# Optimization experiments

Measured on AMD Instinct MI355X. Metric: run time of the kernel, lower is better.

The kernel has to match this reference:

```python
import jax, jax.numpy as jnp
import numpy as np

N = 131072      # nodes decoded per call
LAT, REP, H = 64, 128, 256
FEAT, CEMB, NMAP, CNUM = 512, 128, 101, 27
TEMP = 0.5


def setup_inputs() -> dict:
    key = jax.random.key(0)
    ks = iter(jax.random.split(key, 40))
    w = lambda shape: jax.random.normal(next(ks), shape, jnp.float32) * 0.02
    inp = {
        "z": jax.random.normal(next(ks), (N, LAT), jnp.float32),
        "cluster_ind": jax.random.randint(next(ks), (N,), 0, CNUM),
        "Emb": w((CNUM, CEMB)),
        "Wld": w((LAT, REP)), "bld": w((REP,)),
        "Wrd": w((REP, 3 * H)), "brd": w((3 * H,)),
        "Wfd": w((H, FEAT)), "bfd": w((FEAT,)),
        "Wc1": w((H, H)), "bc1": w((H,)),
        "Wc2": w((H, H)), "bc2": w((H,)),
        "Wc3": w((H, H)), "bc3": w((H,)),
        "Wcd": w((H, CNUM)), "bcd": w((CNUM,)),
        "Wcn": w((CEMB, H)), "bcn": w((H,)),
        "Wnd": w((H, 2 * H)), "bnd": w((2 * H,)),
        "Wn1": w((2 * H, 2 * H)), "bn1": w((2 * H,)),
        "Wn2": w((2 * H, 2 * H)), "bn2": w((2 * H,)),
        "Wa0": w((2 * H, 4 * H)), "ba0": w((4 * H,)),
        "Wa1": w((4 * H, 2 * H)), "ba1": w((2 * H,)),
        "Wn3": w((2 * H, NMAP)), "bn3": w((NMAP,)),
    }
    return inp


def reference(z, cluster_ind, Emb, Wld, bld, Wrd, brd, Wfd, bfd,
              Wc1, bc1, Wc2, bc2, Wc3, bc3, Wcd, bcd, Wcn, bcn,
              Wnd, bnd, Wn1, bn1, Wn2, bn2, Wa0, ba0, Wa1, ba1, Wn3, bn3):
    relu = jax.nn.relu
    # latent -> reparam -> hidden*3, chunked into (feat, neighbor, cluster)
    z1 = relu(z @ Wld + bld)
    z2 = relu(z1 @ Wrd + brd)
    feat_h, nb_h, cl_h = jnp.split(z2, 3, axis=-1)  # each [N, H]
    # feature head
    feat = jax.nn.sigmoid(feat_h @ Wfd + bfd)
    # cluster head
    c = relu(cl_h @ Wc1 + bc1)
    c = relu(c @ Wc2 + bc2)
    c = relu(c @ Wc3 + bc3)
    cluster = jax.nn.sigmoid((c @ Wcd + bcd) / TEMP)
    # neighbor head, conditioned on cluster embedding (training branch)
    emb = Emb[cluster_ind]                      # [N, CEMB]
    ctn = relu(emb @ Wcn + bcn)                 # [N, H]
    nf = relu((nb_h + ctn) @ Wnd + bnd)
    nf = relu(nf @ Wn1 + bn1)
    nf = relu(nf @ Wn2 + bn2)
    nf = relu(nf @ Wa0 + ba0)
    nf = relu(nf @ Wa1 + ba1)
    neighbor_map = jax.nn.sigmoid((nf @ Wn3 + bn3) / TEMP)
    return (feat, neighbor_map, cluster)
```

## Files before the change

kernel.cpp:

```cpp
#include <hip/hip_runtime.h>
#include <hip/hip_bf16.h>

typedef short bf16x8 __attribute__((ext_vector_type(8)));
typedef float f32x4 __attribute__((ext_vector_type(4)));

#define NN 131072
#define BM 128
#define WRS 512
#define SRS 128

#define OFF_LD 0
#define OFF_RD 8192
#define OFF_FD 106496
#define OFF_C1 237568
#define OFF_C2 303104
#define OFF_C3 368640
#define OFF_CD 434176
#define OFF_CN 442368
#define OFF_ND 475136
#define OFF_N1 606208
#define OFF_N2 868352
#define OFF_A0 1130496
#define OFF_A1 1654784
#define OFF_N3 2179072
#define WT_TOTAL 2236416

__device__ __forceinline__ unsigned short f2b(float f) {
  __hip_bfloat16 h = __float2bfloat16(f);
  return __builtin_bit_cast(unsigned short, h);
}
__device__ __forceinline__ float b2f(unsigned short u) {
  return __bfloat162float(__builtin_bit_cast(__hip_bfloat16, u));
}

template<int Kd, int Md>
__device__ __forceinline__ unsigned short convF(int local, const float* __restrict__ W) {
  int block = local >> 9;
  int within = local & 511;
  int lane = within >> 3, j = within & 7;
  constexpr int NK = Kd / 32;
  int ctile = block / NK;
  int kch = block - ctile * NK;
  int col = ctile * 16 + (lane & 15);
  int k = kch * 32 + (lane >> 4) * 8 + j;
  return (col < Md) ? f2b(W[(size_t)k * Md + col]) : (unsigned short)0;
}

__global__ void prep_weights(const float* __restrict__ Wld, const float* __restrict__ Wrd,
                             const float* __restrict__ Wfd, const float* __restrict__ Wc1,
                             const float* __restrict__ Wc2, const float* __restrict__ Wc3,
                             const float* __restrict__ Wcd, const float* __restrict__ Wcn,
                             const float* __restrict__ Wnd, const float* __restrict__ Wn1,
                             const float* __restrict__ Wn2, const float* __restrict__ Wa0,
                             const float* __restrict__ Wa1, const float* __restrict__ Wn3,
                             unsigned short* __restrict__ WT) {
  int e = blockIdx.x * 256 + threadIdx.x;
  unsigned short r;
  if      (e < OFF_RD) r = convF<64, 128>(e - OFF_LD, Wld);
  else if (e < OFF_FD) r = convF<128, 768>(e - OFF_RD, Wrd);
  else if (e < OFF_C1) r = convF<256, 512>(e - OFF_FD, Wfd);
  else if (e < OFF_C2) r = convF<256, 256>(e - OFF_C1, Wc1);
  else if (e < OFF_C3) r = convF<256, 256>(e - OFF_C2, Wc2);
  else if (e < OFF_CD) r = convF<256, 256>(e - OFF_C3, Wc3);
  else if (e < OFF_CN) r = convF<256, 27>(e - OFF_CD, Wcd);
  else if (e < OFF_ND) r = convF<128, 256>(e - OFF_CN, Wcn);
  else if (e < OFF_N1) r = convF<256, 512>(e - OFF_ND, Wnd);
  else if (e < OFF_N2) r = convF<512, 512>(e - OFF_N1, Wn1);
  else if (e < OFF_A0) r = convF<512, 512>(e - OFF_N2, Wn2);
  else if (e < OFF_A1) r = convF<512, 1024>(e - OFF_A0, Wa0);
  else if (e < OFF_N3) r = convF<1024, 512>(e - OFF_A1, Wa1);
  else                 r = convF<512, 101>(e - OFF_N3, Wn3);
  WT[e] = r;
}

template<int K, int NOUT, int GSIZE, int ACT, bool TO_GLOBAL, bool ADD>
__device__ __forceinline__ void layer(
    const unsigned short* __restrict__ Ain, int ars,
    const unsigned short* __restrict__ Bw,
    const float* __restrict__ bias,
    unsigned short* __restrict__ Lout, int ors,
    float* __restrict__ Gout, int gld,
    const unsigned short* __restrict__ Aadd, int rsa,
    int lane, int wid) {
  constexpr int NS = K / 32;
  constexpr int NT = (NOUT + 15) >> 4;
  constexpr int NG = (NT + GSIZE - 1) / GSIZE;
  const int l15 = lane & 15;
  const int quad = lane >> 4;
  const int kh = quad << 3;
  const int sw = (l15 & 7) << 3;
  const unsigned short* a0b = Ain + l15 * ars;
  const unsigned short* a1b = Ain + (64 + l15) * ars;
  #pragma unroll 1
  for (int g = wid; g < NG; g += 8) {
    f32x4 acc[8][GSIZE] = {};
    const unsigned short* bp[GSIZE];
    #pragma unroll
    for (int t = 0; t < GSIZE; ++t)
      bp[t] = Bw + (size_t)(g * GSIZE + t) * (NS * 512) + lane * 8;
    __builtin_amdgcn_s_setprio(1);
    #pragma unroll 2
    for (int s = 0; s < NS; ++s) {
      bf16x8 bb[GSIZE];
      #pragma unroll
      for (int t = 0; t < GSIZE; ++t) bb[t] = *(const bf16x8*)(bp[t] + s * 512);
      int kx = (kh + s * 32) ^ sw;
      #pragma unroll
      for (int m = 0; m < 8; ++m) {
        bf16x8 a = *(const bf16x8*)((m < 4 ? a0b : a1b) + (m & 3) * 16 * ars + kx);
        #pragma unroll
        for (int t = 0; t < GSIZE; ++t)
          acc[m][t] = __builtin_amdgcn_mfma_f32_16x16x32_bf16(a, bb[t], acc[m][t], 0, 0, 0);
      }
    }
    __builtin_amdgcn_s_setprio(0);
    #pragma unroll
    for (int t = 0; t < GSIZE; ++t) {
      int col = (g * GSIZE + t) * 16 + l15;
      int cc = col < NOUT ? col : NOUT - 1;
      float bb2 = bias[cc];
      #pragma unroll
      for (int m = 0; m < 8; ++m) {
        #pragma unroll
        for (int j = 0; j < 4; ++j) {
          int row = m * 16 + quad * 4 + j;
          int rsw = (row & 7) << 3;
          float v = acc[m][t][j] + bb2;
          if constexpr (ACT == 0) v = fmaxf(v, 0.f);
          else if constexpr (ACT == 1) v = 1.f / (1.f + __expf(-v));
          else if constexpr (ACT == 2) v = 1.f / (1.f + __expf(-2.f * v));
          if constexpr (ADD) v += b2f(Aadd[row * rsa + (col ^ rsw)]);
          if constexpr (TO_GLOBAL) {
            if (col < NOUT) Gout[(size_t)row * gld + col] = v;
          } else {
            Lout[row * ors + (col ^ rsw)] = f2b(v);
          }
        }
      }
    }
  }
}

template<int K>
__device__ __forceinline__ void layer512_ip(
    unsigned short* __restrict__ Wb,
    const unsigned short* __restrict__ Bw, const float* __restrict__ bias,
    int lane, int wid) {
  constexpr int NS = K / 32;
  const int l15 = lane & 15;
  const int quad = lane >> 4;
  const int kh = quad << 3;
  const int sw = (l15 & 7) << 3;
  f32x4 acc[8][4] = {};
  const unsigned short* bp[4];
  #pragma unroll
  for (int t = 0; t < 4; ++t)
    bp[t] = Bw + (size_t)(wid * 4 + t) * (NS * 512) + lane * 8;
  const unsigned short* a0b = Wb + l15 * WRS;
  const unsigned short* a1b = Wb + (64 + l15) * WRS;
  __builtin_amdgcn_s_setprio(1);
  #pragma unroll 2
  for (int s = 0; s < NS; ++s) {
    bf16x8 bb[4];
    #pragma unroll
    for (int t = 0; t < 4; ++t) bb[t] = *(const bf16x8*)(bp[t] + s * 512);
    int kx = (kh + s * 32) ^ sw;
    #pragma unroll
    for (int m = 0; m < 8; ++m) {
      bf16x8 a = *(const bf16x8*)((m < 4 ? a0b : a1b) + (m & 3) * 16 * WRS + kx);
      #pragma unroll
      for (int t = 0; t < 4; ++t)
        acc[m][t] = __builtin_amdgcn_mfma_f32_16x16x32_bf16(a, bb[t], acc[m][t], 0, 0, 0);
    }
  }
  __builtin_amdgcn_s_setprio(0);
  __syncthreads();
  #pragma unroll
  for (int t = 0; t < 4; ++t) {
    int col = wid * 64 + t * 16 + l15;
    float bb2 = bias[col];
    #pragma unroll
    for (int m = 0; m < 8; ++m) {
      #pragma unroll
      for (int j = 0; j < 4; ++j) {
        int row = m * 16 + quad * 4 + j;
        Wb[row * WRS + (col ^ ((row & 7) << 3))] = f2b(fmaxf(acc[m][t][j] + bb2, 0.f));
      }
    }
  }
  __syncthreads();
}

__global__ __launch_bounds__(512, 2)
void fused_vae(const float* __restrict__ z, const int* __restrict__ cind,
               const float* __restrict__ Emb,
               const float* __restrict__ bld, const float* __restrict__ brd,
               const float* __restrict__ bfd, const float* __restrict__ bc1,
               const float* __restrict__ bc2, const float* __restrict__ bc3,
               const float* __restrict__ bcd, const float* __restrict__ bcn,
               const float* __restrict__ bnd, const float* __restrict__ bn1,
               const float* __restrict__ bn2, const float* __restrict__ ba0,
               const float* __restrict__ ba1, const float* __restrict__ bn3,
               const unsigned short* __restrict__ WT, float* __restrict__ out) {
  __shared__ unsigned short lds[BM * (WRS + SRS)];
  unsigned short* Wb = lds;
  unsigned short* Sb = lds + BM * WRS;
  const int tid = threadIdx.x;
  const int lane = tid & 63;
  const int wid = tid >> 6;
  const size_t row0 = (size_t)blockIdx.x * BM;

  for (int e = tid * 4; e < BM * 64; e += 512 * 4) {
    int r = e >> 6, c = e & 63;
    float4 v = *(const float4*)(z + (row0 + r) * 64 + c);
    ushort4 u; u.x = f2b(v.x); u.y = f2b(v.y); u.z = f2b(v.z); u.w = f2b(v.w);
    *(ushort4*)(&Wb[r * WRS + (c ^ ((r & 7) << 3))]) = u;
  }
  __syncthreads();
  layer<64, 128, 1, 0, false, false>(Wb, WRS, WT + OFF_LD, bld, Sb, SRS, nullptr, 0, nullptr, 0, lane, wid);
  __syncthreads();
  layer<128, 256, 2, 0, false, false>(Sb, SRS, WT + OFF_RD + (size_t)32 * 4 * 512, brd + 512, Wb, WRS, nullptr, 0, nullptr, 0, lane, wid);
  __syncthreads();
  layer<256, 256, 2, 0, false, false>(Wb, WRS, WT + OFF_C1, bc1, Wb + 256, WRS, nullptr, 0, nullptr, 0, lane, wid);
  __syncthreads();
  layer<256, 256, 2, 0, false, false>(Wb + 256, WRS, WT + OFF_C2, bc2, Wb, WRS, nullptr, 0, nullptr, 0, lane, wid);
  __syncthreads();
  layer<256, 256, 2, 0, false, false>(Wb, WRS, WT + OFF_C3, bc3, Wb + 256, WRS, nullptr, 0, nullptr, 0, lane, wid);
  __syncthreads();
  layer<256, 27, 1, 2, true, false>(Wb + 256, WRS, WT + OFF_CD, bcd, nullptr, 0,
                                    out + (size_t)NN * 613 + row0 * 27, 27, nullptr, 0, lane, wid);
  layer<128, 256, 2, 0, false, false>(Sb, SRS, WT + OFF_RD, brd, Wb, WRS, nullptr, 0, nullptr, 0, lane, wid);
  __syncthreads();
  layer<256, 512, 2, 1, true, false>(Wb, WRS, WT + OFF_FD, bfd, nullptr, 0,
                                     out + row0 * 512, 512, nullptr, 0, lane, wid);
  layer<128, 256, 2, 0, false, false>(Sb, SRS, WT + OFF_RD + (size_t)16 * 4 * 512, brd + 256, Wb + 256, WRS, nullptr, 0, nullptr, 0, lane, wid);
  __syncthreads();
  for (int e = tid * 4; e < BM * 128; e += 512 * 4) {
    int r = e >> 7, c = e & 127;
    int ci = cind[row0 + r];
    float4 v = *(const float4*)(Emb + (size_t)ci * 128 + c);
    ushort4 u; u.x = f2b(v.x); u.y = f2b(v.y); u.z = f2b(v.z); u.w = f2b(v.w);
    *(ushort4*)(&Sb[r * SRS + (c ^ ((r & 7) << 3))]) = u;
  }
  __syncthreads();
  layer<128, 256, 2, 0, false, true>(Sb, SRS, WT + OFF_CN, bcn, Wb, WRS, nullptr, 0, Wb + 256, WRS, lane, wid);
  __syncthreads();
  layer512_ip<256>(Wb, WT + OFF_ND, bnd, lane, wid);
  layer512_ip<512>(Wb, WT + OFF_N1, bn1, lane, wid);
  layer512_ip<512>(Wb, WT + OFF_N2, bn2, lane, wid);
  {
    const int l15 = lane & 15;
    const int quad = lane >> 4;
    const int kh = quad << 3;
    const int sw = (l15 & 7) << 3;
    #pragma unroll 1
    for (int rh = 0; rh < 2; ++rh) {
      f32x4 acc1[4][4] = {};
      const unsigned short* awb = Wb + (rh * 64 + l15) * WRS;
      #pragma unroll 1
      for (int e = 0; e < 8; ++e) {
        unsigned short* sbuf = Sb + (e & 1) * (64 * SRS);
        f32x4 acc0[4] = {};
        const unsigned short* bp = WT + OFF_A0 + (size_t)(e * 8 + wid) * (16 * 512) + lane * 8;
        __builtin_amdgcn_s_setprio(1);
        #pragma unroll 2
        for (int s = 0; s < 16; ++s) {
          bf16x8 b = *(const bf16x8*)(bp + s * 512);
          int kx = (kh + s * 32) ^ sw;
          #pragma unroll
          for (int m = 0; m < 4; ++m) {
            bf16x8 a = *(const bf16x8*)(awb + m * 16 * WRS + kx);
            acc0[m] = __builtin_amdgcn_mfma_f32_16x16x32_bf16(a, b, acc0[m], 0, 0, 0);
          }
        }
        __builtin_amdgcn_s_setprio(0);
        {
          int lc = wid * 16 + l15;
          float bb2 = ba0[e * 128 + lc];
          #pragma unroll
          for (int m = 0; m < 4; ++m) {
            #pragma unroll
            for (int j = 0; j < 4; ++j) {
              int row = m * 16 + quad * 4 + j;
              sbuf[row * SRS + (lc ^ ((row & 7) << 3))] = f2b(fmaxf(acc0[m][j] + bb2, 0.f));
            }
          }
        }
        __syncthreads();
        const unsigned short* asb = sbuf + l15 * SRS;
        const unsigned short* bp1[4];
        #pragma unroll
        for (int t = 0; t < 4; ++t)
          bp1[t] = WT + OFF_A1 + (size_t)(wid * 4 + t) * (32 * 512) + (size_t)(e * 4) * 512 + lane * 8;
        __builtin_amdgcn_s_setprio(1);
        #pragma unroll
        for (int s = 0; s < 4; ++s) {
          bf16x8 b[4];
          #pragma unroll
          for (int t = 0; t < 4; ++t) b[t] = *(const bf16x8*)(bp1[t] + s * 512);
          int kx = (kh + s * 32) ^ sw;
          #pragma unroll
          for (int m = 0; m < 4; ++m) {
            bf16x8 a = *(const bf16x8*)(asb + m * 16 * SRS + kx);
            #pragma unroll
            for (int t = 0; t < 4; ++t)
              acc1[m][t] = __builtin_amdgcn_mfma_f32_16x16x32_bf16(a, b[t], acc1[m][t], 0, 0, 0);
          }
        }
        __builtin_amdgcn_s_setprio(0);
      }
      #pragma unroll
      for (int t = 0; t < 4; ++t) {
        int col = wid * 64 + t * 16 + l15;
        float bb2 = ba1[col];
        #pragma unroll
        for (int m = 0; m < 4; ++m) {
          #pragma unroll
          for (int j = 0; j < 4; ++j) {
            int row = rh * 64 + m * 16 + quad * 4 + j;
            Wb[row * WRS + (col ^ ((row & 7) << 3))] = f2b(fmaxf(acc1[m][t][j] + bb2, 0.f));
          }
        }
      }
    }
  }
  __syncthreads();
  layer<512, 101, 1, 2, true, false>(Wb, WRS, WT + OFF_N3, bn3, nullptr, 0,
                                     out + (size_t)NN * 512 + row0 * 101, 101, nullptr, 0, lane, wid);
}

extern "C" void kernel_launch(void* const* d_in, const int* in_sizes, int n_in,
                              void* d_out, int out_size, void* d_ws, size_t ws_size,
                              hipStream_t stream) {
  const float* z   = (const float*)d_in[0];
  const int*   cind= (const int*)d_in[1];
  const float* Emb = (const float*)d_in[2];
  const float* Wld = (const float*)d_in[3];  const float* bld = (const float*)d_in[4];
  const float* Wrd = (const float*)d_in[5];  const float* brd = (const float*)d_in[6];
  const float* Wfd = (const float*)d_in[7];  const float* bfd = (const float*)d_in[8];
  const float* Wc1 = (const float*)d_in[9];  const float* bc1 = (const float*)d_in[10];
  const float* Wc2 = (const float*)d_in[11]; const float* bc2 = (const float*)d_in[12];
  const float* Wc3 = (const float*)d_in[13]; const float* bc3 = (const float*)d_in[14];
  const float* Wcd = (const float*)d_in[15]; const float* bcd = (const float*)d_in[16];
  const float* Wcn = (const float*)d_in[17]; const float* bcn = (const float*)d_in[18];
  const float* Wnd = (const float*)d_in[19]; const float* bnd = (const float*)d_in[20];
  const float* Wn1 = (const float*)d_in[21]; const float* bn1 = (const float*)d_in[22];
  const float* Wn2 = (const float*)d_in[23]; const float* bn2 = (const float*)d_in[24];
  const float* Wa0 = (const float*)d_in[25]; const float* ba0 = (const float*)d_in[26];
  const float* Wa1 = (const float*)d_in[27]; const float* ba1 = (const float*)d_in[28];
  const float* Wn3 = (const float*)d_in[29]; const float* bn3 = (const float*)d_in[30];
  unsigned short* WT = (unsigned short*)d_ws;
  float* out = (float*)d_out;

  prep_weights<<<WT_TOTAL / 256, 256, 0, stream>>>(Wld, Wrd, Wfd, Wc1, Wc2, Wc3, Wcd,
                                                   Wcn, Wnd, Wn1, Wn2, Wa0, Wa1, Wn3, WT);
  fused_vae<<<NN / BM, 512, 0, stream>>>(z, cind, Emb, bld, brd, bfd, bc1, bc2, bc3,
                                         bcd, bcn, bnd, bn1, bn2, ba0, ba1, bn3, WT, out);
}
```

Measured before the change: 740.6 us.

## Split warps across row halves and widen column groups to cut weight reloads

The 8 warps are reorganized into 4 column groups by 2 row halves. Each warp now computes 64 rows by a wider set of output tiles (GSIZE doubled), so B-weight fragments loaded from global are reused across more MFMAs per A load. The fused A0/A1 MLP loop now processes 256-column chunks in 4 iterations with a single 64x256 staging buffer and an extra barrier, in place of 8 double-buffered 128-column chunks. This trades more accumulator registers and different LDS access patterns for fewer global weight fetches and fewer synchronisations.

```diff
diff --git a/kernel.cpp b/kernel.cpp
--- a/kernel.cpp
+++ b/kernel.cpp
@@ -85,19 +85,23 @@
   constexpr int NS = K / 32;
   constexpr int NT = (NOUT + 15) >> 4;
   constexpr int NG = (NT + GSIZE - 1) / GSIZE;
+  const int cg = wid >> 1;
+  const int rbase = (wid & 1) * 64;
   const int l15 = lane & 15;
   const int quad = lane >> 4;
   const int kh = quad << 3;
   const int sw = (l15 & 7) << 3;
-  const unsigned short* a0b = Ain + l15 * ars;
-  const unsigned short* a1b = Ain + (64 + l15) * ars;
+  const unsigned short* ab = Ain + (rbase + l15) * ars;
   #pragma unroll 1
-  for (int g = wid; g < NG; g += 8) {
-    f32x4 acc[8][GSIZE] = {};
+  for (int g = cg; g < NG; g += 4) {
+    f32x4 acc[4][GSIZE] = {};
     const unsigned short* bp[GSIZE];
     #pragma unroll
-    for (int t = 0; t < GSIZE; ++t)
-      bp[t] = Bw + (size_t)(g * GSIZE + t) * (NS * 512) + lane * 8;
+    for (int t = 0; t < GSIZE; ++t) {
+      int ti = g * GSIZE + t;
+      int tc = ti < NT ? ti : NT - 1;
+      bp[t] = Bw + (size_t)tc * (NS * 512) + lane * 8;
+    }
     __builtin_amdgcn_s_setprio(1);
     #pragma unroll 2
     for (int s = 0; s < NS; ++s) {
@@ -106,8 +110,8 @@
       for (int t = 0; t < GSIZE; ++t) bb[t] = *(const bf16x8*)(bp[t] + s * 512);
       int kx = (kh + s * 32) ^ sw;
       #pragma unroll
-      for (int m = 0; m < 8; ++m) {
-        bf16x8 a = *(const bf16x8*)((m < 4 ? a0b : a1b) + (m & 3) * 16 * ars + kx);
+      for (int m = 0; m < 4; ++m) {
+        bf16x8 a = *(const bf16x8*)(ab + m * 16 * ars + kx);
         #pragma unroll
         for (int t = 0; t < GSIZE; ++t)
           acc[m][t] = __builtin_amdgcn_mfma_f32_16x16x32_bf16(a, bb[t], acc[m][t], 0, 0, 0);
@@ -120,10 +124,10 @@
       int cc = col < NOUT ? col : NOUT - 1;
       float bb2 = bias[cc];
       #pragma unroll
-      for (int m = 0; m < 8; ++m) {
+      for (int m = 0; m < 4; ++m) {
         #pragma unroll
         for (int j = 0; j < 4; ++j) {
-          int row = m * 16 + quad * 4 + j;
+          int row = rbase + m * 16 + quad * 4 + j;
           int rsw = (row & 7) << 3;
           float v = acc[m][t][j] + bb2;
           if constexpr (ACT == 0) v = fmaxf(v, 0.f);
@@ -147,43 +151,41 @@
     const unsigned short* __restrict__ Bw, const float* __restrict__ bias,
     int lane, int wid) {
   constexpr int NS = K / 32;
+  const int cg = wid >> 1;
+  const int rbase = (wid & 1) * 64;
   const int l15 = lane & 15;
   const int quad = lane >> 4;
   const int kh = quad << 3;
   const int sw = (l15 & 7) << 3;
-  f32x4 acc[8][4] = {};
-  const unsigned short* bp[4];
-  #pragma unroll
-  for (int t = 0; t < 4; ++t)
-    bp[t] = Bw + (size_t)(wid * 4 + t) * (NS * 512) + lane * 8;
-  const unsigned short* a0b = Wb + l15 * WRS;
-  const unsigned short* a1b = Wb + (64 + l15) * WRS;
+  f32x4 acc[4][8] = {};
+  const unsigned short* bp = Bw + (size_t)(cg * 8) * (NS * 512) + lane * 8;
+  const unsigned short* ab = Wb + (rbase + l15) * WRS;
   __builtin_amdgcn_s_setprio(1);
   #pragma unroll 2
   for (int s = 0; s < NS; ++s) {
-    bf16x8 bb[4];
-    #pragma unroll
-    for (int t = 0; t < 4; ++t) bb[t] = *(const bf16x8*)(bp[t] + s * 512);
+    bf16x8 bb[8];
+    #pragma unroll
+    for (int t = 0; t < 8; ++t) bb[t] = *(const bf16x8*)(bp + (size_t)t * (NS * 512) + s * 512);
     int kx = (kh + s * 32) ^ sw;
     #pragma unroll
-    for (int m = 0; m < 8; ++m) {
-      bf16x8 a = *(const bf16x8*)((m < 4 ? a0b : a1b) + (m & 3) * 16 * WRS + kx);
-      #pragma unroll
-      for (int t = 0; t < 4; ++t)
+    for (int m = 0; m < 4; ++m) {
+      bf16x8 a = *(const bf16x8*)(ab + m * 16 * WRS + kx);
+      #pragma unroll
+      for (int t = 0; t < 8; ++t)
         acc[m][t] = __builtin_amdgcn_mfma_f32_16x16x32_bf16(a, bb[t], acc[m][t], 0, 0, 0);
     }
   }
   __builtin_amdgcn_s_setprio(0);
   __syncthreads();
   #pragma unroll
-  for (int t = 0; t < 4; ++t) {
-    int col = wid * 64 + t * 16 + l15;
+  for (int t = 0; t < 8; ++t) {
+    int col = cg * 128 + t * 16 + l15;
     float bb2 = bias[col];
     #pragma unroll
-    for (int m = 0; m < 8; ++m) {
+    for (int m = 0; m < 4; ++m) {
       #pragma unroll
       for (int j = 0; j < 4; ++j) {
-        int row = m * 16 + quad * 4 + j;
+        int row = rbase + m * 16 + quad * 4 + j;
         Wb[row * WRS + (col ^ ((row & 7) << 3))] = f2b(fmaxf(acc[m][t][j] + bb2, 0.f));
       }
     }
@@ -217,23 +219,23 @@
     *(ushort4*)(&Wb[r * WRS + (c ^ ((r & 7) << 3))]) = u;
   }
   __syncthreads();
-  layer<64, 128, 1, 0, false, false>(Wb, WRS, WT + OFF_LD, bld, Sb, SRS, nullptr, 0, nullptr, 0, lane, wid);
-  __syncthreads();
-  layer<128, 256, 2, 0, false, false>(Sb, SRS, WT + OFF_RD + (size_t)32 * 4 * 512, brd + 512, Wb, WRS, nullptr, 0, nullptr, 0, lane, wid);
-  __syncthreads();
-  layer<256, 256, 2, 0, false, false>(Wb, WRS, WT + OFF_C1, bc1, Wb + 256, WRS, nullptr, 0, nullptr, 0, lane, wid);
-  __syncthreads();
-  layer<256, 256, 2, 0, false, false>(Wb + 256, WRS, WT + OFF_C2, bc2, Wb, WRS, nullptr, 0, nullptr, 0, lane, wid);
-  __syncthreads();
-  layer<256, 256, 2, 0, false, false>(Wb, WRS, WT + OFF_C3, bc3, Wb + 256, WRS, nullptr, 0, nullptr, 0, lane, wid);
+  layer<64, 128, 2, 0, false, false>(Wb, WRS, WT + OFF_LD, bld, Sb, SRS, nullptr, 0, nullptr, 0, lane, wid);
+  __syncthreads();
+  layer<128, 256, 4, 0, false, false>(Sb, SRS, WT + OFF_RD + (size_t)32 * 4 * 512, brd + 512, Wb, WRS, nullptr, 0, nullptr, 0, lane, wid);
+  __syncthreads();
+  layer<256, 256, 4, 0, false, false>(Wb, WRS, WT + OFF_C1, bc1, Wb + 256, WRS, nullptr, 0, nullptr, 0, lane, wid);
+  __syncthreads();
+  layer<256, 256, 4, 0, false, false>(Wb + 256, WRS, WT + OFF_C2, bc2, Wb, WRS, nullptr, 0, nullptr, 0, lane, wid);
+  __syncthreads();
+  layer<256, 256, 4, 0, false, false>(Wb, WRS, WT + OFF_C3, bc3, Wb + 256, WRS, nullptr, 0, nullptr, 0, lane, wid);
   __syncthreads();
   layer<256, 27, 1, 2, true, false>(Wb + 256, WRS, WT + OFF_CD, bcd, nullptr, 0,
                                     out + (size_t)NN * 613 + row0 * 27, 27, nullptr, 0, lane, wid);
-  layer<128, 256, 2, 0, false, false>(Sb, SRS, WT + OFF_RD, brd, Wb, WRS, nullptr, 0, nullptr, 0, lane, wid);
-  __syncthreads();
-  layer<256, 512, 2, 1, true, false>(Wb, WRS, WT + OFF_FD, bfd, nullptr, 0,
+  layer<128, 256, 4, 0, false, false>(Sb, SRS, WT + OFF_RD, brd, Wb, WRS, nullptr, 0, nullptr, 0, lane, wid);
+  __syncthreads();
+  layer<256, 512, 4, 1, true, false>(Wb, WRS, WT + OFF_FD, bfd, nullptr, 0,
                                      out + row0 * 512, 512, nullptr, 0, lane, wid);
-  layer<128, 256, 2, 0, false, false>(Sb, SRS, WT + OFF_RD + (size_t)16 * 4 * 512, brd + 256, Wb + 256, WRS, nullptr, 0, nullptr, 0, lane, wid);
+  layer<128, 256, 4, 0, false, false>(Sb, SRS, WT + OFF_RD + (size_t)16 * 4 * 512, brd + 256, Wb + 256, WRS, nullptr, 0, nullptr, 0, lane, wid);
   __syncthreads();
   for (int e = tid * 4; e < BM * 128; e += 512 * 4) {
     int r = e >> 7, c = e & 127;
@@ -243,7 +245,7 @@
     *(ushort4*)(&Sb[r * SRS + (c ^ ((r & 7) << 3))]) = u;
   }
   __syncthreads();
-  layer<128, 256, 2, 0, false, true>(Sb, SRS, WT + OFF_CN, bcn, Wb, WRS, nullptr, 0, Wb + 256, WRS, lane, wid);
+  layer<128, 256, 4, 0, false, true>(Sb, SRS, WT + OFF_CN, bcn, Wb, WRS, nullptr, 0, Wb + 256, WRS, lane, wid);
   __syncthreads();
   layer512_ip<256>(Wb, WT + OFF_ND, bnd, lane, wid);
   layer512_ip<512>(Wb, WT + OFF_N1, bn1, lane, wid);
@@ -257,51 +259,51 @@
     for (int rh = 0; rh < 2; ++rh) {
       f32x4 acc1[4][4] = {};
       const unsigned short* awb = Wb + (rh * 64 + l15) * WRS;
+      const unsigned short* asb = Sb + l15 * 256;
       #pragma unroll 1
-      for (int e = 0; e < 8; ++e) {
-        unsigned short* sbuf = Sb + (e & 1) * (64 * SRS);
-        f32x4 acc0[4] = {};
-        const unsigned short* bp = WT + OFF_A0 + (size_t)(e * 8 + wid) * (16 * 512) + lane * 8;
+      for (int e = 0; e < 4; ++e) {
+        f32x4 acc0[4][2] = {};
+        const unsigned short* bp0 = WT + OFF_A0 + (size_t)(e * 16 + wid * 2) * (16 * 512) + lane * 8;
         __builtin_amdgcn_s_setprio(1);
         #pragma unroll 2
         for (int s = 0; s < 16; ++s) {
-          bf16x8 b = *(const bf16x8*)(bp + s * 512);
+          bf16x8 b0 = *(const bf16x8*)(bp0 + s * 512);
+          bf16x8 b1 = *(const bf16x8*)(bp0 + 16 * 512 + s * 512);
           int kx = (kh + s * 32) ^ sw;
           #pragma unroll
           for (int m = 0; m < 4; ++m) {
             bf16x8 a = *(const bf16x8*)(awb + m * 16 * WRS + kx);
-            acc0[m] = __builtin_amdgcn_mfma_f32_16x16x32_bf16(a, b, acc0[m], 0, 0, 0);
+            acc0[m][0] = __builtin_amdgcn_mfma_f32_16x16x32_bf16(a, b0, acc0[m][0], 0, 0, 0);
+            acc0[m][1] = __builtin_amdgcn_mfma_f32_16x16x32_bf16(a, b1, acc0[m][1], 0, 0, 0);
           }
         }
         __builtin_amdgcn_s_setprio(0);
-        {
-          int lc = wid * 16 + l15;
-          float bb2 = ba0[e * 128 + lc];
+        __syncthreads();
+        #pragma unroll
+        for (int t = 0; t < 2; ++t) {
+          int lc = wid * 32 + t * 16 + l15;
+          float bb2 = ba0[e * 256 + lc];
           #pragma unroll
           for (int m = 0; m < 4; ++m) {
             #pragma unroll
             for (int j = 0; j < 4; ++j) {
               int row = m * 16 + quad * 4 + j;
-              sbuf[row * SRS + (lc ^ ((row & 7) << 3))] = f2b(fmaxf(acc0[m][j] + bb2, 0.f));
+              Sb[row * 256 + (lc ^ ((row & 7) << 3))] = f2b(fmaxf(acc0[m][t][j] + bb2, 0.f));
             }
           }
         }
         __syncthreads();
-        const unsigned short* asb = sbuf + l15 * SRS;
-        const unsigned short* bp1[4];
-        #pragma unroll
-        for (int t = 0; t < 4; ++t)
-          bp1[t] = WT + OFF_A1 + (size_t)(wid * 4 + t) * (32 * 512) + (size_t)(e * 4) * 512 + lane * 8;
+        const unsigned short* bp1 = WT + OFF_A1 + (size_t)(wid * 4) * (32 * 512) + (size_t)(e * 8) * 512 + lane * 8;
         __builtin_amdgcn_s_setprio(1);
-        #pragma unroll
-        for (int s = 0; s < 4; ++s) {
+        #pragma unroll 2
+        for (int s = 0; s < 8; ++s) {
           bf16x8 b[4];
           #pragma unroll
-          for (int t = 0; t < 4; ++t) b[t] = *(const bf16x8*)(bp1[t] + s * 512);
+          for (int t = 0; t < 4; ++t) b[t] = *(const bf16x8*)(bp1 + (size_t)t * (32 * 512) + s * 512);
           int kx = (kh + s * 32) ^ sw;
           #pragma unroll
           for (int m = 0; m < 4; ++m) {
-            bf16x8 a = *(const bf16x8*)(asb + m * 16 * SRS + kx);
+            bf16x8 a = *(const bf16x8*)(asb + m * 16 * 256 + kx);
             #pragma unroll
             for (int t = 0; t < 4; ++t)
               acc1[m][t] = __builtin_amdgcn_mfma_f32_16x16x32_bf16(a, b[t], acc1[m][t], 0, 0, 0);
@@ -325,7 +327,7 @@
     }
   }
   __syncthreads();
-  layer<512, 101, 1, 2, true, false>(Wb, WRS, WT + OFF_N3, bn3, nullptr, 0,
+  layer<512, 101, 2, 2, true, false>(Wb, WRS, WT + OFF_N3, bn3, nullptr, 0,
                                      out + (size_t)NN * 512 + row0 * 101, 101, nullptr, 0, lane, wid);
 }
 
```

Measured after the change: 660.9 us, median of 2. 1.12x faster.
